# Optimization experiments

Measured on AMD Instinct MI355X. Metric: run time of the kernel, lower is better.

The kernel has to match this reference:

```python
import jax, jax.numpy as jnp
import numpy as np

STRIDE, PADDING, EPS = 2, 1, 1e-5


def setup_inputs() -> dict:
    key = jax.random.key(0)
    k1, k2, k3 = jax.random.split(key, 3)
    C_in, C_out, K = 64, 64, 4
    x = jax.random.normal(k1, (32, C_in, 64, 64), dtype=jnp.float32)
    weight = jax.random.normal(k2, (C_in, C_out, K, K), dtype=jnp.float32) * 0.05  # torch layout (in,out,kh,kw)
    conv_bias = jax.random.normal(k3, (C_out,), dtype=jnp.float32) * 0.02
    gamma = jnp.ones((C_out,), dtype=jnp.float32)
    beta = jnp.zeros((C_out,), dtype=jnp.float32)
    running_mean = jnp.zeros((C_out,), dtype=jnp.float32)
    running_var = jnp.ones((C_out,), dtype=jnp.float32)
    return {"x": x, "weight": weight, "conv_bias": conv_bias, "gamma": gamma,
            "beta": beta, "running_mean": running_mean, "running_var": running_var}


def _conv_transpose2d(x, weight, bias, stride, padding):
    # torch.nn.functional.conv_transpose2d equivalent:
    # conv with lhs_dilation=stride, spatially-flipped kernel, in/out axes swapped,
    # and padding k-1-p on each side.
    k = weight.shape[2]
    w_t = jnp.transpose(jnp.flip(weight, (2, 3)), (1, 0, 2, 3))  # (Cout, Cin, k, k)
    pad = k - 1 - padding
    y = jax.lax.conv_general_dilated(
        x, w_t,
        window_strides=(1, 1),
        padding=[(pad, pad), (pad, pad)],
        lhs_dilation=(stride, stride),
        dimension_numbers=("NCHW", "OIHW", "NCHW"),
    )
    return y + bias[None, :, None, None]


def reference(x, weight, conv_bias, gamma, beta, running_mean, running_var):
    # ConvTranspose2d
    y = _conv_transpose2d(x, weight, conv_bias, STRIDE, PADDING)  # [N,C,128,128]
    # BatchNorm2d (inference, running stats)
    scale = gamma * jax.lax.rsqrt(running_var + EPS)
    y = (y - running_mean[None, :, None, None]) * scale[None, :, None, None] + beta[None, :, None, None]
    # Softmax over channel dim
    y = jax.nn.softmax(y, axis=1)
    # MaxPool2d(k=2, s=2): H,W are even, so reshape-max is exact
    N, C, H, W = y.shape
    y = y.reshape(N, C, H // 2, 2, W // 2, 2).max(axis=(3, 5))  # [N,C,64,64]
    return y
```

## Files before the change

### kernel.cpp

```cpp
#include <hip/hip_runtime.h>
#include <math.h>


typedef __attribute__((ext_vector_type(8))) short short8;
typedef __attribute__((ext_vector_type(4))) float floatx4;

#define COLS 66

__device__ ushort g_wfrag[4 * 8 * 4 * 64 * 8];
__device__ float g_aff[128];

__device__ __forceinline__ ushort f2bf(float f) {
  union { float f; unsigned u; } v; v.f = f;
  unsigned r = v.u + 0x7FFF + ((v.u >> 16) & 1);
  return (ushort)(r >> 16);
}

__global__ __launch_bounds__(256) void prep_kernel(
    const float* __restrict__ w, const float* __restrict__ bias,
    const float* __restrict__ gamma, const float* __restrict__ beta,
    const float* __restrict__ mean, const float* __restrict__ var) {
  int t = blockIdx.x * 256 + threadIdx.x;
  int cin0 = (t >> 6) * 2;
  int cout = t & 63;
  int nt = cout >> 4, b15 = cout & 15;
  int q = (cin0 & 31) >> 3;
  int j = cin0 & 7;
  int ksq = cin0 >> 5;

  const float4* p0 = (const float4*)&w[(cin0 * 64 + cout) * 16];
  const float4* p1 = (const float4*)&w[((cin0 + 1) * 64 + cout) * 16];
  float a[16], b[16];
  {
    float4 f0 = p0[0], f1 = p0[1], f2 = p0[2], f3 = p0[3];
    a[0]=f0.x; a[1]=f0.y; a[2]=f0.z; a[3]=f0.w; a[4]=f1.x; a[5]=f1.y; a[6]=f1.z; a[7]=f1.w;
    a[8]=f2.x; a[9]=f2.y; a[10]=f2.z; a[11]=f2.w; a[12]=f3.x; a[13]=f3.y; a[14]=f3.z; a[15]=f3.w;
    float4 g0 = p1[0], g1 = p1[1], g2 = p1[2], g3 = p1[3];
    b[0]=g0.x; b[1]=g0.y; b[2]=g0.z; b[3]=g0.w; b[4]=g1.x; b[5]=g1.y; b[6]=g1.z; b[7]=g1.w;
    b[8]=g2.x; b[9]=g2.y; b[10]=g2.z; b[11]=g2.w; b[12]=g3.x; b[13]=g3.y; b[14]=g3.z; b[15]=g3.w;
  }
#pragma unroll
  for (int kh = 0; kh < 4; ++kh)
#pragma unroll
    for (int kw = 0; kw < 4; ++kw) {
      int r = (kh & 1) ? 0 : 1;
      int pp = (kw & 1) ? 0 : 1;
      int c = r * 2 + pp;
      int tap = (kh >> 1) * 2 + (kw >> 1);
      int ks = tap * 2 + ksq;
      unsigned u = (unsigned)f2bf(a[kh * 4 + kw]) | ((unsigned)f2bf(b[kh * 4 + kw]) << 16);
      *(unsigned*)&g_wfrag[(((c * 8 + ks) * 4 + nt) * 64 + q * 16 + b15) * 8 + j] = u;
    }

  if (t < 64) {
    float A = gamma[t] * rsqrtf(var[t] + 1e-5f);
    g_aff[t] = A;
    g_aff[64 + t] = (bias[t] - mean[t]) * A + beta[t];
  }
}

__global__ __launch_bounds__(256, 4) void fused_kernel(const float* __restrict__ x,
                                                       float* __restrict__ out) {
  __shared__ ushort xs[4 * COLS * 64];

  const int tid  = threadIdx.x;
  const int ph0  = blockIdx.x * 2;
  const int n    = blockIdx.y;
  const int wave = tid >> 6;
  const int lane = tid & 63;
  const int b15  = lane & 15;
  const int q    = lane >> 4;
  const int wr   = wave >> 1;
  const int wc   = wave & 1;

  for (int e = tid; e < 4 * 16 * 32; e += 256) {
    int iw2 = e & 31;
    int c4  = (e >> 5) & 15;
    int row = e >> 9;
    int ih  = ph0 - 1 + row;
    float2 v0 = {0.f, 0.f}, v1 = v0, v2 = v0, v3 = v0;
    if (ih >= 0 && ih < 64) {
      const float* xp = x + ((n * 64 + c4 * 4) * 64 + ih) * 64 + iw2 * 2;
      v0 = *(const float2*)xp;          v1 = *(const float2*)(xp + 4096);
      v2 = *(const float2*)(xp + 8192); v3 = *(const float2*)(xp + 12288);
    }
    int chunk = c4 >> 1, half4 = (c4 & 1) * 4;
    {
      int col = iw2 * 2 + 1;
      ushort4 pk; pk.x = f2bf(v0.x); pk.y = f2bf(v1.x); pk.z = f2bf(v2.x); pk.w = f2bf(v3.x);
      *(ushort4*)&xs[(row * COLS + col) * 64 + ((chunk ^ (col & 7)) * 8) + half4] = pk;
    }
    {
      int col = iw2 * 2 + 2;
      ushort4 pk; pk.x = f2bf(v0.y); pk.y = f2bf(v1.y); pk.z = f2bf(v2.y); pk.w = f2bf(v3.y);
      *(ushort4*)&xs[(row * COLS + col) * 64 + ((chunk ^ (col & 7)) * 8) + half4] = pk;
    }
  }
  for (int e = tid; e < 4 * 2 * 16; e += 256) {
    int c4 = e & 15, side = (e >> 4) & 1, row = e >> 5;
    int col = side ? 65 : 0;
    int chunk = c4 >> 1, half4 = (c4 & 1) * 4;
    ushort4 z; z.x = z.y = z.z = z.w = 0;
    *(ushort4*)&xs[(row * COLS + col) * 64 + ((chunk ^ (col & 7)) * 8) + half4] = z;
  }
  __syncthreads();

  float Ac[4], Dc[4];
#pragma unroll
  for (int nt = 0; nt < 4; ++nt) {
    Ac[nt] = g_aff[nt * 16 + b15];
    Dc[nt] = g_aff[64 + nt * 16 + b15];
  }

  floatx4 pooled[8];
#pragma unroll
  for (int i = 0; i < 8; ++i) pooled[i] = (floatx4){0.f, 0.f, 0.f, 0.f};

  for (int c = 0; c < 4; ++c) {
    const int r = c >> 1, p = c & 1;
    floatx4 acc[8];
#pragma unroll
    for (int i = 0; i < 8; ++i) acc[i] = (floatx4){0.f, 0.f, 0.f, 0.f};

#pragma unroll
    for (int ks = 0; ks < 8; ++ks) {
      const int tap = ks >> 1, a = tap >> 1, b = tap & 1;
      const int hrow = wr + (r ? (a ? 1 : 2) : (a ? 0 : 1));
      const int dx   = p ? (b ? 0 : 1) : (b ? -1 : 0);
      const int chunk = (ks & 1) * 4 + q;
      const short8* wf = (const short8*)&g_wfrag[((c * 8 + ks) * 4) * 512];
      short8 bf[4];
#pragma unroll
      for (int nt = 0; nt < 4; ++nt) bf[nt] = wf[nt * 64 + lane];
      short8 af[2];
#pragma unroll
      for (int mt = 0; mt < 2; ++mt) {
        int col = wc * 32 + mt * 16 + b15 + dx + 1;
        af[mt] = *(const short8*)&xs[(hrow * COLS + col) * 64 + ((chunk ^ (col & 7)) * 8)];
      }
#pragma unroll
      for (int nt = 0; nt < 4; ++nt)
#pragma unroll
        for (int mt = 0; mt < 2; ++mt)
          acc[mt * 4 + nt] =
              __builtin_amdgcn_mfma_f32_16x16x32_bf16(af[mt], bf[nt], acc[mt * 4 + nt], 0, 0, 0);
    }

#pragma unroll
    for (int mt = 0; mt < 2; ++mt) {
      float v[16];
      float sm[4] = {0.f, 0.f, 0.f, 0.f};
#pragma unroll
      for (int nt = 0; nt < 4; ++nt)
#pragma unroll
        for (int reg = 0; reg < 4; ++reg) {
          float e = __expf(fmaf(acc[mt * 4 + nt][reg], Ac[nt], Dc[nt]));
          v[nt * 4 + reg] = e;
          sm[reg] += e;
        }
#pragma unroll
      for (int reg = 0; reg < 4; ++reg) {
        sm[reg] += __shfl_xor(sm[reg], 1, 64);
        sm[reg] += __shfl_xor(sm[reg], 2, 64);
        sm[reg] += __shfl_xor(sm[reg], 4, 64);
        sm[reg] += __shfl_xor(sm[reg], 8, 64);
        sm[reg] = 1.0f / sm[reg];
      }
#pragma unroll
      for (int nt = 0; nt < 4; ++nt)
#pragma unroll
        for (int reg = 0; reg < 4; ++reg)
          pooled[mt * 4 + nt][reg] =
              fmaxf(pooled[mt * 4 + nt][reg], v[nt * 4 + reg] * sm[reg]);
    }
  }

  __syncthreads();
  float* red = (float*)xs;
#pragma unroll
  for (int mt = 0; mt < 2; ++mt)
#pragma unroll
    for (int nt = 0; nt < 4; ++nt)
#pragma unroll
      for (int reg = 0; reg < 4; ++reg)
        red[(wr * 64 + nt * 16 + b15) * 66 + wc * 32 + mt * 16 + q * 4 + reg] =
            pooled[mt * 4 + nt][reg];
  __syncthreads();
  for (int e = tid; e < 4096; e += 256) {
    int pw2  = e & 31;
    int cout = (e >> 5) & 63;
    int rl   = e >> 11;
    float2 val = *(float2*)&red[(rl * 64 + cout) * 66 + pw2 * 2];
    *(float2*)&out[((n * 64 + cout) * 64 + (ph0 + rl)) * 64 + pw2 * 2] = val;
  }
}

extern "C" void kernel_launch(void* const* d_in, const int* in_sizes, int n_in,
                              void* d_out, int out_size, void* d_ws, size_t ws_size,
                              hipStream_t stream) {
  const float* x     = (const float*)d_in[0];
  const float* w     = (const float*)d_in[1];
  const float* bias  = (const float*)d_in[2];
  const float* gamma = (const float*)d_in[3];
  const float* beta  = (const float*)d_in[4];
  const float* mean  = (const float*)d_in[5];
  const float* var   = (const float*)d_in[6];
  float* out = (float*)d_out;

  prep_kernel<<<8, 256, 0, stream>>>(w, bias, gamma, beta, mean, var);
  dim3 grid(32, 32);
  fused_kernel<<<grid, 256, 0, stream>>>(x, out);
}
```

Baseline: 122.1 us.

## Fold BN scale into weights, widen x loads, double-buffer weight fragments

Folds the BatchNorm scale into the bf16 weight fragments during prep, so the epilogue only adds a per-channel shift before exp. The x staging loop now reads float4 and converts with packed bf16 intrinsics, halving the load iterations. Weight fragments for the next k-step are prefetched into a second register set while the current MFMAs run, and the softmax reuses the accumulator registers instead of a separate array. Rounding the scaled weights to bf16 changes numerics slightly, and the double buffer raises register pressure under the 4-blocks-per-CU launch bound.

```diff
diff --git a/kernel.cpp b/kernel.cpp
--- a/kernel.cpp
+++ b/kernel.cpp
@@ -1,4 +1,5 @@
 #include <hip/hip_runtime.h>
+#include <hip/hip_bf16.h>
 #include <math.h>
 
 
@@ -8,7 +9,7 @@
 #define COLS 66
 
 __device__ ushort g_wfrag[4 * 8 * 4 * 64 * 8];
-__device__ float g_aff[128];
+__device__ float g_aff[64];
 
 __device__ __forceinline__ ushort f2bf(float f) {
   union { float f; unsigned u; } v; v.f = f;
@@ -27,6 +28,7 @@
   int q = (cin0 & 31) >> 3;
   int j = cin0 & 7;
   int ksq = cin0 >> 5;
+  float A = gamma[cout] * rsqrtf(var[cout] + 1e-5f);
 
   const float4* p0 = (const float4*)&w[(cin0 * 64 + cout) * 16];
   const float4* p1 = (const float4*)&w[((cin0 + 1) * 64 + cout) * 16];
@@ -48,14 +50,14 @@
       int c = r * 2 + pp;
       int tap = (kh >> 1) * 2 + (kw >> 1);
       int ks = tap * 2 + ksq;
-      unsigned u = (unsigned)f2bf(a[kh * 4 + kw]) | ((unsigned)f2bf(b[kh * 4 + kw]) << 16);
+      unsigned u = (unsigned)f2bf(a[kh * 4 + kw] * A) |
+                   ((unsigned)f2bf(b[kh * 4 + kw] * A) << 16);
       *(unsigned*)&g_wfrag[(((c * 8 + ks) * 4 + nt) * 64 + q * 16 + b15) * 8 + j] = u;
     }
 
   if (t < 64) {
-    float A = gamma[t] * rsqrtf(var[t] + 1e-5f);
-    g_aff[t] = A;
-    g_aff[64 + t] = (bias[t] - mean[t]) * A + beta[t];
+    float Ai = gamma[t] * rsqrtf(var[t] + 1e-5f);
+    g_aff[t] = (bias[t] - mean[t]) * Ai + beta[t];
   }
 }
 
@@ -73,26 +75,26 @@
   const int wr   = wave >> 1;
   const int wc   = wave & 1;
 
-  for (int e = tid; e < 4 * 16 * 32; e += 256) {
-    int iw2 = e & 31;
-    int c4  = (e >> 5) & 15;
-    int row = e >> 9;
+  for (int e = tid; e < 4 * 16 * 16; e += 256) {
+    int iw4 = e & 15;
+    int c4  = (e >> 4) & 15;
+    int row = e >> 8;
     int ih  = ph0 - 1 + row;
-    float2 v0 = {0.f, 0.f}, v1 = v0, v2 = v0, v3 = v0;
+    float4 v0 = {0.f, 0.f, 0.f, 0.f}, v1 = v0, v2 = v0, v3 = v0;
     if (ih >= 0 && ih < 64) {
-      const float* xp = x + ((n * 64 + c4 * 4) * 64 + ih) * 64 + iw2 * 2;
-      v0 = *(const float2*)xp;          v1 = *(const float2*)(xp + 4096);
-      v2 = *(const float2*)(xp + 8192); v3 = *(const float2*)(xp + 12288);
+      const float* xp = x + ((n * 64 + c4 * 4) * 64 + ih) * 64 + iw4 * 4;
+      v0 = *(const float4*)xp;          v1 = *(const float4*)(xp + 4096);
+      v2 = *(const float4*)(xp + 8192); v3 = *(const float4*)(xp + 12288);
     }
     int chunk = c4 >> 1, half4 = (c4 & 1) * 4;
-    {
-      int col = iw2 * 2 + 1;
-      ushort4 pk; pk.x = f2bf(v0.x); pk.y = f2bf(v1.x); pk.z = f2bf(v2.x); pk.w = f2bf(v3.x);
-      *(ushort4*)&xs[(row * COLS + col) * 64 + ((chunk ^ (col & 7)) * 8) + half4] = pk;
-    }
-    {
-      int col = iw2 * 2 + 2;
-      ushort4 pk; pk.x = f2bf(v0.y); pk.y = f2bf(v1.y); pk.z = f2bf(v2.y); pk.w = f2bf(v3.y);
+    float cc[4][4] = {{v0.x, v1.x, v2.x, v3.x}, {v0.y, v1.y, v2.y, v3.y},
+                      {v0.z, v1.z, v2.z, v3.z}, {v0.w, v1.w, v2.w, v3.w}};
+#pragma unroll
+    for (int ii = 0; ii < 4; ++ii) {
+      int col = iw4 * 4 + ii + 1;
+      __hip_bfloat162 lo = __float22bfloat162_rn({cc[ii][0], cc[ii][1]});
+      __hip_bfloat162 hi = __float22bfloat162_rn({cc[ii][2], cc[ii][3]});
+      ushort4 pk = {*(ushort*)&lo.x, *(ushort*)&lo.y, *(ushort*)&hi.x, *(ushort*)&hi.y};
       *(ushort4*)&xs[(row * COLS + col) * 64 + ((chunk ^ (col & 7)) * 8) + half4] = pk;
     }
   }
@@ -105,16 +107,20 @@
   }
   __syncthreads();
 
-  float Ac[4], Dc[4];
-#pragma unroll
-  for (int nt = 0; nt < 4; ++nt) {
-    Ac[nt] = g_aff[nt * 16 + b15];
-    Dc[nt] = g_aff[64 + nt * 16 + b15];
-  }
+  float Dc[4];
+#pragma unroll
+  for (int nt = 0; nt < 4; ++nt) Dc[nt] = g_aff[nt * 16 + b15];
 
   floatx4 pooled[8];
 #pragma unroll
   for (int i = 0; i < 8; ++i) pooled[i] = (floatx4){0.f, 0.f, 0.f, 0.f};
+
+  short8 bfA[4], bfB[4];
+  {
+    const short8* wf = (const short8*)g_wfrag;
+#pragma unroll
+    for (int nt = 0; nt < 4; ++nt) bfA[nt] = wf[nt * 64 + lane];
+  }
 
   for (int c = 0; c < 4; ++c) {
     const int r = c >> 1, p = c & 1;
@@ -124,14 +130,21 @@
 
 #pragma unroll
     for (int ks = 0; ks < 8; ++ks) {
-      const int tap = ks >> 1, a = tap >> 1, b = tap & 1;
+      short8* cur = (ks & 1) ? bfB : bfA;
+      short8* nxt = (ks & 1) ? bfA : bfB;
+      if (ks < 7) {
+        const short8* wf = (const short8*)g_wfrag + (c * 8 + ks + 1) * 256;
+#pragma unroll
+        for (int nt = 0; nt < 4; ++nt) nxt[nt] = wf[nt * 64 + lane];
+      } else if (c < 3) {
+        const short8* wf = (const short8*)g_wfrag + (c + 1) * 8 * 256;
+#pragma unroll
+        for (int nt = 0; nt < 4; ++nt) nxt[nt] = wf[nt * 64 + lane];
+      }
+      const int a = ks >> 2, b = (ks >> 1) & 1;
       const int hrow = wr + (r ? (a ? 1 : 2) : (a ? 0 : 1));
       const int dx   = p ? (b ? 0 : 1) : (b ? -1 : 0);
       const int chunk = (ks & 1) * 4 + q;
-      const short8* wf = (const short8*)&g_wfrag[((c * 8 + ks) * 4) * 512];
-      short8 bf[4];
-#pragma unroll
-      for (int nt = 0; nt < 4; ++nt) bf[nt] = wf[nt * 64 + lane];
       short8 af[2];
 #pragma unroll
       for (int mt = 0; mt < 2; ++mt) {
@@ -143,19 +156,18 @@
 #pragma unroll
         for (int mt = 0; mt < 2; ++mt)
           acc[mt * 4 + nt] =
-              __builtin_amdgcn_mfma_f32_16x16x32_bf16(af[mt], bf[nt], acc[mt * 4 + nt], 0, 0, 0);
+              __builtin_amdgcn_mfma_f32_16x16x32_bf16(af[mt], cur[nt], acc[mt * 4 + nt], 0, 0, 0);
     }
 
 #pragma unroll
     for (int mt = 0; mt < 2; ++mt) {
-      float v[16];
       float sm[4] = {0.f, 0.f, 0.f, 0.f};
 #pragma unroll
       for (int nt = 0; nt < 4; ++nt)
 #pragma unroll
         for (int reg = 0; reg < 4; ++reg) {
-          float e = __expf(fmaf(acc[mt * 4 + nt][reg], Ac[nt], Dc[nt]));
-          v[nt * 4 + reg] = e;
+          float e = __expf(acc[mt * 4 + nt][reg] + Dc[nt]);
+          acc[mt * 4 + nt][reg] = e;
           sm[reg] += e;
         }
 #pragma unroll
@@ -171,7 +183,7 @@
 #pragma unroll
         for (int reg = 0; reg < 4; ++reg)
           pooled[mt * 4 + nt][reg] =
-              fmaxf(pooled[mt * 4 + nt][reg], v[nt * 4 + reg] * sm[reg]);
+              fmaxf(pooled[mt * 4 + nt][reg], acc[mt * 4 + nt][reg] * sm[reg]);
     }
   }
 
```

After: 120.8 us. About the same (-1.1%).
